# Kernel optimization log

Measured on AMD Instinct MI355X. Metric: run time of the kernel, lower is better.

Reference implementation:

```python
import jax, jax.numpy as jnp
import numpy as np
from jax.ops import segment_sum, segment_max

N_NODES = 100000
N_EDGES = 3200000
NODE_FEAT = 128
EDGE_DIM = 8
H = 4          # heads for all three layers
C_HID = 8      # out_layer_1 == out_layer_2 == 8
N_CLASSES = 1
NEG_SLOPE = 0.2


def setup_inputs() -> dict:
    key = jax.random.key(0)
    ks = jax.random.split(key, 20)
    g = lambda k, shape, fan: jax.random.normal(k, shape, jnp.float32) / np.sqrt(fan)
    inp = {
        "x": jax.random.normal(ks[0], (N_NODES, NODE_FEAT), jnp.float32),
        "edge_attr": jax.random.normal(ks[1], (N_EDGES, EDGE_DIM), jnp.float32),
        "edge_index": jax.random.randint(ks[2], (2, N_EDGES), 0, N_NODES, jnp.int32),
        # layer 1: node_feat -> H*C_HID, concat=True, with edge features
        "W1": g(ks[3], (NODE_FEAT, H * C_HID), NODE_FEAT),
        "a_src1": g(ks[4], (H, C_HID), C_HID),
        "a_dst1": g(ks[5], (H, C_HID), C_HID),
        "We1": g(ks[6], (EDGE_DIM, H * C_HID), EDGE_DIM),
        "a_e1": g(ks[7], (H, C_HID), C_HID),
        "b1": jnp.zeros((H * C_HID,), jnp.float32),
        # layer 2: H*C_HID -> C_HID, concat=False
        "W2": g(ks[8], (H * C_HID, H * C_HID), H * C_HID),
        "a_src2": g(ks[9], (H, C_HID), C_HID),
        "a_dst2": g(ks[10], (H, C_HID), C_HID),
        "b2": jnp.zeros((C_HID,), jnp.float32),
        # layer 3: C_HID -> N_CLASSES, concat=False
        "W3": g(ks[11], (C_HID, H * N_CLASSES), C_HID),
        "a_src3": g(ks[12], (H, N_CLASSES), 1),
        "a_dst3": g(ks[13], (H, N_CLASSES), 1),
        "b3": jnp.zeros((N_CLASSES,), jnp.float32),
    }
    return inp


def _gat_conv(x, src, dst, W, a_src, a_dst, bias, concat,
              edge_attr=None, W_edge=None, a_edge=None):
    """PyG GATConv forward (eval mode). src/dst already include self-loops."""
    n = x.shape[0]
    h, c = a_src.shape
    xh = (x @ W).reshape(n, h, c)                       # [N,H,C]
    alpha = (xh * a_src[None]).sum(-1)[src] \
          + (xh * a_dst[None]).sum(-1)[dst]             # [E,H]
    if edge_attr is not None:
        eh = (edge_attr @ W_edge).reshape(-1, h, c)     # [E,H,C]
        alpha = alpha + (eh * a_edge[None]).sum(-1)
    alpha = jax.nn.leaky_relu(alpha, NEG_SLOPE)
    # segment softmax over incoming edges of each dst node
    amax = segment_max(alpha, dst, num_segments=n)       # [N,H]
    ex = jnp.exp(alpha - amax[dst])
    denom = segment_sum(ex, dst, num_segments=n)
    alpha = ex / (denom[dst] + 1e-16)                    # [E,H]
    out = segment_sum(alpha[:, :, None] * xh[src], dst, num_segments=n)  # [N,H,C]
    out = out.reshape(n, h * c) if concat else out.mean(axis=1)
    return out + bias


def _add_self_loops(edge_index, n):
    loop = jnp.arange(n, dtype=edge_index.dtype)
    src = jnp.concatenate([edge_index[0], loop])
    dst = jnp.concatenate([edge_index[1], loop])
    return src, dst


def reference(x, edge_attr, edge_index, W1, a_src1, a_dst1, We1, a_e1, b1,
              W2, a_src2, a_dst2, b2, W3, a_src3, a_dst3, b3):
    n = x.shape[0]
    src, dst = _add_self_loops(edge_index, n)
    # self-loop edge_attr: fill_value='mean' => scatter-mean of edge_attr by dst
    deg = segment_sum(jnp.ones((edge_index.shape[1],), x.dtype), edge_index[1],
                      num_segments=n)
    mean_attr = segment_sum(edge_attr, edge_index[1], num_segments=n) \
              / jnp.maximum(deg, 1.0)[:, None]
    ea = jnp.concatenate([edge_attr, mean_attr], axis=0)

    h = _gat_conv(x, src, dst, W1, a_src1, a_dst1, b1, True,
                  edge_attr=ea, W_edge=We1, a_edge=a_e1)
    h = jax.nn.elu(h)
    h = _gat_conv(h, src, dst, W2, a_src2, a_dst2, b2, False)
    h = jax.nn.elu(h)
    out = _gat_conv(h, src, dst, W3, a_src3, a_dst3, b3, False)
    return out
```

## Files before the change

### kernel.cpp

```cpp
#include <hip/hip_runtime.h>
#include <hip/hip_fp16.h>
#include <cmath>

static inline int cdiv(long a, int b){ return (int)((a + b - 1) / b); }

__device__ __forceinline__ float lrelu(float x){ return x > 0.f ? x : 0.2f * x; }
__device__ __forceinline__ float elu1(float x){ return x > 0.f ? x : expm1f(x); }
__device__ __forceinline__ float fexp(float x){ return __expf(x); }
__device__ __forceinline__ float sel4(float4 v, int h){
  float ab = (h & 1) ? v.y : v.x;
  float cd = (h & 1) ? v.w : v.z;
  return (h & 2) ? cd : ab;
}

#define WAVE_FENCE() do { asm volatile("" ::: "memory"); __builtin_amdgcn_sched_barrier(0); } while(0)

#define W_SHIFT 7
#define BUCKET_N (1 << W_SHIFT)
#define NBMAX   1024
#define NCHUNKS 1024
#define CH_MAX  3136
#define MS_THREADS 1024



__global__ __launch_bounds__(MS_THREADS)
void hist_chunks_kernel(const int* __restrict__ ei, int E, int CH, int* __restrict__ hist2d){
  __shared__ int s_b[NBMAX];
  int t = threadIdx.x, chunk = blockIdx.x;
  s_b[t] = 0;
  __syncthreads();
  int lo = chunk * CH, hi = min(lo + CH, E);
  for (int e = lo + t; e < hi; e += MS_THREADS)
    atomicAdd(&s_b[ei[E + e] >> W_SHIFT], 1);
  __syncthreads();
  hist2d[(size_t)chunk * NBMAX + t] = s_b[t];
}

__global__ __launch_bounds__(NCHUNKS)
void col_scan_kernel(int* __restrict__ hist2d, int* __restrict__ bcnt){
  __shared__ int s[NCHUNKS];
  int b = blockIdx.x, t = threadIdx.x;
  int v = hist2d[(size_t)t * NBMAX + b];
  s[t] = v; __syncthreads();
  #pragma unroll
  for (int off = 1; off < NCHUNKS; off <<= 1){
    int u = (t >= off) ? s[t - off] : 0;
    __syncthreads();
    s[t] += u;
    __syncthreads();
  }
  hist2d[(size_t)t * NBMAX + b] = s[t] - v;
  if (t == NCHUNKS - 1) bcnt[b] = s[t];
}

__global__ void scan_buckets_kernel(const int* __restrict__ bcnt, int nb, int total,
                                    int* __restrict__ bstart, int* __restrict__ row_start, int n){
  __shared__ int s[1024];
  int t = threadIdx.x;
  int v = (t < nb) ? bcnt[t] : 0;
  s[t] = v; __syncthreads();
  #pragma unroll
  for (int off = 1; off < 1024; off <<= 1){
    int u = (t >= off) ? s[t - off] : 0;
    __syncthreads();
    s[t] += u;
    __syncthreads();
  }
  bstart[t] = (t < nb) ? s[t] - v : total;
  if (t == 0){ bstart[NBMAX] = total; row_start[n] = total; }
}

__global__ void wevec_kernel(const float* __restrict__ We, const float* __restrict__ ae,
                             float* __restrict__ wev){
  int i = threadIdx.x;
  if (i >= 32) return;
  int d = i >> 2, h = i & 3;
  float acc = 0.f;
  #pragma unroll
  for (int c = 0; c < 8; ++c) acc = fmaf(We[d * 32 + h * 8 + c], ae[h * 8 + c], acc);
  wev[d * 4 + h] = acc;
}

__global__ __launch_bounds__(MS_THREADS)
void multisplit_kernel(const int* __restrict__ ei, int E, int CH,
                       const float* __restrict__ eattr, const float* __restrict__ wev,
                       const int* __restrict__ bstart, const int* __restrict__ prefix2d,
                       int4* __restrict__ staged){
  __shared__ int4 s_rec[CH_MAX];
  __shared__ int s_fill[NBMAX];
  __shared__ int s_lbase[NBMAX];
  __shared__ int s_shift[NBMAX];
  __shared__ float s_wev[32];
  int t = threadIdx.x, chunk = blockIdx.x;
  if (t < 32) s_wev[t] = wev[t];
  s_fill[t] = 0;
  __syncthreads();
  int lo = chunk * CH, hi = min(lo + CH, E);
  int cnt = hi - lo;
  for (int e = lo + t; e < hi; e += MS_THREADS)
    atomicAdd(&s_fill[ei[E + e] >> W_SHIFT], 1);
  __syncthreads();
  int v = s_fill[t];
  s_lbase[t] = v; __syncthreads();
  #pragma unroll
  for (int off = 1; off < NBMAX; off <<= 1){
    int u = (t >= off) ? s_lbase[t - off] : 0;
    __syncthreads();
    s_lbase[t] += u;
    __syncthreads();
  }
  int excl = s_lbase[t] - v;
  s_lbase[t] = excl;
  s_shift[t] = bstart[t] + prefix2d[(size_t)chunk * NBMAX + t] - excl;
  s_fill[t] = 0;
  __syncthreads();
  for (int e = lo + t; e < hi; e += MS_THREADS){
    int d = ei[E + e];
    int b = d >> W_SHIFT;
    const float4* ea = (const float4*)(eattr + (size_t)e * 8);
    float4 v0 = ea[0], v1 = ea[1];
    float av[8] = {v0.x, v0.y, v0.z, v0.w, v1.x, v1.y, v1.z, v1.w};
    float e0 = 0, e1 = 0, e2 = 0, e3 = 0;
    #pragma unroll
    for (int k = 0; k < 8; ++k){
      e0 = fmaf(av[k], s_wev[k * 4 + 0], e0);
      e1 = fmaf(av[k], s_wev[k * 4 + 1], e1);
      e2 = fmaf(av[k], s_wev[k * 4 + 2], e2);
      e3 = fmaf(av[k], s_wev[k * 4 + 3], e3);
    }
    __half2 h01 = __floats2half2_rn(e0, e1);
    __half2 h23 = __floats2half2_rn(e2, e3);
    int pos = s_lbase[b] + atomicAdd(&s_fill[b], 1);
    s_rec[pos] = make_int4(ei[e], d,
                           __builtin_bit_cast(int, h01), __builtin_bit_cast(int, h23));
  }
  __syncthreads();
  for (int i = t; i < cnt; i += MS_THREADS){
    int4 r = s_rec[i];
    staged[s_shift[r.y >> W_SHIFT] + i] = r;
  }
}

__global__ __launch_bounds__(MS_THREADS)
void bucket_scatter_kernel(const int* __restrict__ bstart, const int4* __restrict__ staged,
                           int n, int* __restrict__ row_start, int* __restrict__ srcs,
                           uint2* __restrict__ escp, float4* __restrict__ selfesc){
  __shared__ int s_cnt[BUCKET_N];
  __shared__ int s_cur[BUCKET_N];
  __shared__ int s_start[BUCKET_N];
  int b = blockIdx.x, t = threadIdx.x;
  int node0 = b << W_SHIFT;
  if (t < BUCKET_N) s_cnt[t] = 0;
  __syncthreads();
  int lo = bstart[b], hi = bstart[b + 1];
  for (int i = lo + t; i < hi; i += MS_THREADS)
    atomicAdd(&s_cnt[staged[i].y & (BUCKET_N - 1)], 1);
  __syncthreads();
  if (t < BUCKET_N) s_cur[t] = s_cnt[t];
  __syncthreads();
  #pragma unroll
  for (int off = 1; off < BUCKET_N; off <<= 1){
    int v = (t < BUCKET_N && t >= off) ? s_cur[t - off] : 0;
    __syncthreads();
    if (t < BUCKET_N) s_cur[t] += v;
    __syncthreads();
  }
  if (t < BUCKET_N){
    int excl = s_cur[t] - s_cnt[t];
    int nd = node0 + t;
    if (nd <= n) row_start[nd] = lo + excl;
    s_start[t] = lo + excl;
    s_cur[t] = lo + excl;
  }
  __syncthreads();
  for (int i = lo + t; i < hi; i += MS_THREADS){
    int4 r = staged[i];
    int pos = atomicAdd(&s_cur[r.y & (BUCKET_N - 1)], 1);
    srcs[pos] = r.x;
    escp[pos] = make_uint2((unsigned)r.z, (unsigned)r.w);
  }
  __syncthreads();
  int nl = t >> 3, sub = t & 7;
  int nd2 = node0 + nl;
  if (nd2 >= n) return;
  int r0 = s_start[nl], r1 = s_start[nl] + s_cnt[nl];
  float e0 = 0, e1 = 0, e2 = 0, e3 = 0;
  for (int k = r0 + sub; k < r1; k += 8){
    uint2 u = escp[k];
    float2 f01 = __half22float2(__builtin_bit_cast(__half2, u.x));
    float2 f23 = __half22float2(__builtin_bit_cast(__half2, u.y));
    e0 += f01.x; e1 += f01.y; e2 += f23.x; e3 += f23.y;
  }
  #pragma unroll
  for (int off = 1; off < 8; off <<= 1){
    e0 += __shfl_xor(e0, off, 64); e1 += __shfl_xor(e1, off, 64);
    e2 += __shfl_xor(e2, off, 64); e3 += __shfl_xor(e3, off, 64);
  }
  if (sub == 0){
    float inv = 1.f / fmaxf((float)s_cnt[nl], 1.f);
    selfesc[nd2] = make_float4(e0 * inv, e1 * inv, e2 * inv, e3 * inv);
  }
}

template<int K, int M, int C>
__global__ void gemm_score_kernel(const float* __restrict__ A, const float* __restrict__ W,
                                  const float* __restrict__ asrc, const float* __restrict__ adst,
                                  float* __restrict__ out, float* __restrict__ sS,
                                  float* __restrict__ sD, int n){
  __shared__ float Ws[K * M];
  __shared__ float s_as[M], s_ad[M];
  for (int i = threadIdx.x; i < K * M; i += blockDim.x) Ws[i] = W[i];
  if (threadIdx.x < M){ s_as[threadIdx.x] = asrc[threadIdx.x]; s_ad[threadIdx.x] = adst[threadIdx.x]; }
  __syncthreads();
  constexpr int ROWS = 256 / M;
  int row = blockIdx.x * ROWS + (int)threadIdx.x / M;
  int col = (int)threadIdx.x % M;
  if (row >= n) return;
  const float4* a4 = (const float4*)(A + (size_t)row * K);
  float acc = 0.f;
  #pragma unroll
  for (int k4 = 0; k4 < K / 4; ++k4){
    float4 av = a4[k4];
    acc = fmaf(av.x, Ws[(k4 * 4 + 0) * M + col], acc);
    acc = fmaf(av.y, Ws[(k4 * 4 + 1) * M + col], acc);
    acc = fmaf(av.z, Ws[(k4 * 4 + 2) * M + col], acc);
    acc = fmaf(av.w, Ws[(k4 * 4 + 3) * M + col], acc);
  }
  out[(size_t)row * M + col] = acc;
  float ps = acc * s_as[col], pd = acc * s_ad[col];
  #pragma unroll
  for (int off = 1; off < C; off <<= 1){
    ps += __shfl_xor(ps, off, 64);
    pd += __shfl_xor(pd, off, 64);
  }
  if ((col & (C - 1)) == 0){
    int h = col / C;
    sS[(size_t)row * 4 + h] = ps;
    sD[(size_t)row * 4 + h] = pd;
  }
}

template<int MODE, bool EDGE>
__global__ void gather_kernel(const int* __restrict__ row_start, const int* __restrict__ srcs,
                              const uint2* __restrict__ escp, const float4* __restrict__ selfesc,
                              const float* __restrict__ sS, const float* __restrict__ sD,
                              const float* __restrict__ xh, const float* __restrict__ bias,
                              float* __restrict__ out, int n,
                              const float* __restrict__ W3p, const float* __restrict__ as3p,
                              const float* __restrict__ ad3p, float* __restrict__ xh3,
                              float* __restrict__ ss3, float* __restrict__ sd3){
  int wv = threadIdx.x >> 6, lane = threadIdx.x & 63;
  int node = blockIdx.x * 4 + wv;

  if constexpr (MODE == 2){
    if (node >= n) return;
    int rs = row_start[node], deg = row_start[node + 1] - rs;
    float4 sd4 = ((const float4*)sD)[node];
    float4 acc = {0,0,0,0}, dsum = {0,0,0,0};
    for (int k = lane; k < deg; k += 64){
      int s = srcs[rs + k];
      float4 ss = ((const float4*)sS)[s];
      float4 w;
      w.x = fexp(lrelu(ss.x + sd4.x)); w.y = fexp(lrelu(ss.y + sd4.y));
      w.z = fexp(lrelu(ss.z + sd4.z)); w.w = fexp(lrelu(ss.w + sd4.w));
      dsum.x += w.x; dsum.y += w.y; dsum.z += w.z; dsum.w += w.w;
      float4 xv = ((const float4*)xh)[s];
      acc.x = fmaf(w.x, xv.x, acc.x); acc.y = fmaf(w.y, xv.y, acc.y);
      acc.z = fmaf(w.z, xv.z, acc.z); acc.w = fmaf(w.w, xv.w, acc.w);
    }
    #pragma unroll
    for (int off = 1; off < 64; off <<= 1){
      acc.x += __shfl_xor(acc.x, off, 64); acc.y += __shfl_xor(acc.y, off, 64);
      acc.z += __shfl_xor(acc.z, off, 64); acc.w += __shfl_xor(acc.w, off, 64);
      dsum.x += __shfl_xor(dsum.x, off, 64); dsum.y += __shfl_xor(dsum.y, off, 64);
      dsum.z += __shfl_xor(dsum.z, off, 64); dsum.w += __shfl_xor(dsum.w, off, 64);
    }
    if (lane == 0){
      float4 ssn = ((const float4*)sS)[node];
      float4 wsf;
      wsf.x = fexp(lrelu(ssn.x + sd4.x)); wsf.y = fexp(lrelu(ssn.y + sd4.y));
      wsf.z = fexp(lrelu(ssn.z + sd4.z)); wsf.w = fexp(lrelu(ssn.w + sd4.w));
      float4 xvn = ((const float4*)xh)[node];
      float v = (acc.x + wsf.x * xvn.x) / (dsum.x + wsf.x + 1e-16f)
              + (acc.y + wsf.y * xvn.y) / (dsum.y + wsf.y + 1e-16f)
              + (acc.z + wsf.z * xvn.z) / (dsum.z + wsf.z + 1e-16f)
              + (acc.w + wsf.w * xvn.w) / (dsum.w + wsf.w + 1e-16f);
      out[node] = 0.25f * v + bias[0];
    }
    return;
  } else {
  __shared__ float4 s_w[4][64];
  __shared__ int    s_src[4][64];
  __shared__ float  s_w3[32];
  __shared__ float  s_a3[8];
  if constexpr (MODE == 1){
    if (threadIdx.x < 32) s_w3[threadIdx.x] = W3p[threadIdx.x];
    if (threadIdx.x < 8)
      s_a3[threadIdx.x] = (threadIdx.x < 4) ? as3p[threadIdx.x] : ad3p[threadIdx.x - 4];
    __syncthreads();
  }
  if (node >= n) return;
  int rs = row_start[node], deg = row_start[node + 1] - rs;
  float4 sd4 = ((const float4*)sD)[node];
  int q = lane & 7;
  int h = q >> 1;
  int sg = lane >> 3;
  float4 acc = {0,0,0,0};
  float dacc = 0.f;

  for (int base = 0; base < deg; base += 64){
    int k = base + lane;
    float4 w = {0,0,0,0}; int s = 0;
    if (k < deg){
      s = srcs[rs + k];
      float4 ss = ((const float4*)sS)[s];
      float a0 = ss.x + sd4.x, a1 = ss.y + sd4.y, a2 = ss.z + sd4.z, a3 = ss.w + sd4.w;
      if constexpr (EDGE){
        uint2 u = escp[rs + k];
        float2 f01 = __half22float2(__builtin_bit_cast(__half2, u.x));
        float2 f23 = __half22float2(__builtin_bit_cast(__half2, u.y));
        a0 += f01.x; a1 += f01.y; a2 += f23.x; a3 += f23.y;
      }
      w.x = fexp(lrelu(a0)); w.y = fexp(lrelu(a1));
      w.z = fexp(lrelu(a2)); w.w = fexp(lrelu(a3));
    }
    s_w[wv][lane] = w;
    s_src[wv][lane] = s;
    WAVE_FENCE();
    int nvalid = min(deg - base, 64);
    const float* s_wf = (const float*)&s_w[wv][0];
    #pragma unroll
    for (int i = 0; i < 8; ++i){
      int slot = i * 8 + sg;
      if (slot < nvalid){
        int s2 = s_src[wv][slot];
        float wg = s_wf[slot * 4 + h];
        float4 xv = ((const float4*)xh)[(size_t)s2 * 8 + q];
        dacc += wg;
        acc.x = fmaf(wg, xv.x, acc.x); acc.y = fmaf(wg, xv.y, acc.y);
        acc.z = fmaf(wg, xv.z, acc.z); acc.w = fmaf(wg, xv.w, acc.w);
      }
    }
    WAVE_FENCE();
  }

  #pragma unroll
  for (int off = 8; off < 64; off <<= 1){
    acc.x += __shfl_xor(acc.x, off, 64); acc.y += __shfl_xor(acc.y, off, 64);
    acc.z += __shfl_xor(acc.z, off, 64); acc.w += __shfl_xor(acc.w, off, 64);
    dacc  += __shfl_xor(dacc,  off, 64);
  }
  float4 ssn = ((const float4*)sS)[node];
  float a_self = sel4(ssn, h) + sel4(sd4, h);
  if constexpr (EDGE) a_self += sel4(selfesc[node], h);
  float wsel = fexp(lrelu(a_self));
  float4 xvn = ((const float4*)xh)[(size_t)node * 8 + q];
  acc.x = fmaf(wsel, xvn.x, acc.x); acc.y = fmaf(wsel, xvn.y, acc.y);
  acc.z = fmaf(wsel, xvn.z, acc.z); acc.w = fmaf(wsel, xvn.w, acc.w);
  dacc += wsel;
  float rin = 1.f / (dacc + 1e-16f);
  float4 val = {acc.x * rin, acc.y * rin, acc.z * rin, acc.w * rin};

  if constexpr (MODE == 0){
    float4 b4 = ((const float4*)bias)[q];
    val.x = elu1(val.x + b4.x); val.y = elu1(val.y + b4.y);
    val.z = elu1(val.z + b4.z); val.w = elu1(val.w + b4.w);
    if (lane < 8) ((float4*)out)[(size_t)node * 8 + lane] = val;
  } else {
    val.x += __shfl_xor(val.x, 2, 64); val.y += __shfl_xor(val.y, 2, 64);
    val.z += __shfl_xor(val.z, 2, 64); val.w += __shfl_xor(val.w, 2, 64);
    val.x += __shfl_xor(val.x, 4, 64); val.y += __shfl_xor(val.y, 4, 64);
    val.z += __shfl_xor(val.z, 4, 64); val.w += __shfl_xor(val.w, 4, 64);
    float4 b4 = ((const float4*)bias)[q & 1];
    val.x = elu1(val.x * 0.25f + b4.x); val.y = elu1(val.y * 0.25f + b4.y);
    val.z = elu1(val.z * 0.25f + b4.z); val.w = elu1(val.w * 0.25f + b4.w);
    float4 oth;
    oth.x = __shfl_xor(val.x, 1, 64); oth.y = __shfl_xor(val.y, 1, 64);
    oth.z = __shfl_xor(val.z, 1, 64); oth.w = __shfl_xor(val.w, 1, 64);
    float h2v[8];
    if (q & 1){
      h2v[0] = oth.x; h2v[1] = oth.y; h2v[2] = oth.z; h2v[3] = oth.w;
      h2v[4] = val.x; h2v[5] = val.y; h2v[6] = val.z; h2v[7] = val.w;
    } else {
      h2v[0] = val.x; h2v[1] = val.y; h2v[2] = val.z; h2v[3] = val.w;
      h2v[4] = oth.x; h2v[5] = oth.y; h2v[6] = oth.z; h2v[7] = oth.w;
    }
    float x3[4];
    #pragma unroll
    for (int j = 0; j < 4; ++j){
      float a = 0.f;
      #pragma unroll
      for (int k = 0; k < 8; ++k) a = fmaf(h2v[k], s_w3[k * 4 + j], a);
      x3[j] = a;
    }
    if (lane == 0){
      ((float4*)xh3)[node] = make_float4(x3[0], x3[1], x3[2], x3[3]);
      ((float4*)ss3)[node] = make_float4(x3[0] * s_a3[0], x3[1] * s_a3[1],
                                         x3[2] * s_a3[2], x3[3] * s_a3[3]);
      ((float4*)sd3)[node] = make_float4(x3[0] * s_a3[4], x3[1] * s_a3[5],
                                         x3[2] * s_a3[6], x3[3] * s_a3[7]);
    }
  }
  }
}


extern "C" void kernel_launch(void* const* d_in, const int* in_sizes, int n_in,
                              void* d_out, int out_size, void* d_ws, size_t ws_size,
                              hipStream_t stream){
  const float* x     = (const float*)d_in[0];
  const float* eattr = (const float*)d_in[1];
  const int*   ei    = (const int*)d_in[2];
  const float* W1  = (const float*)d_in[3];
  const float* as1 = (const float*)d_in[4];
  const float* ad1 = (const float*)d_in[5];
  const float* We1 = (const float*)d_in[6];
  const float* ae1 = (const float*)d_in[7];
  const float* b1  = (const float*)d_in[8];
  const float* W2  = (const float*)d_in[9];
  const float* as2 = (const float*)d_in[10];
  const float* ad2 = (const float*)d_in[11];
  const float* b2  = (const float*)d_in[12];
  const float* W3  = (const float*)d_in[13];
  const float* as3 = (const float*)d_in[14];
  const float* ad3 = (const float*)d_in[15];
  const float* b3  = (const float*)d_in[16];

  const int N = in_sizes[0] / 128;
  const int E = in_sizes[2] / 2;
  const int nb_buckets = (N + BUCKET_N - 1) >> W_SHIFT;
  const int CH = cdiv(E, NCHUNKS);

  char* b0 = (char*)d_ws;
  int4* staged = (int4*)b0;
  float* fp = (float*)b0;
  float* xh = fp; fp += (size_t)N * 32;
  float* sS = fp; fp += (size_t)N * 4;
  float* sD = fp; fp += (size_t)N * 4;
  float* h1 = fp; fp += (size_t)N * 32;
  int*  srcs = (int*)(b0 + (size_t)E * 16);
  uint2* escp = (uint2*)(b0 + (size_t)E * 20);
  int* hist2d = (int*)(b0 + (size_t)E * 28);
  float4* selfesc = (float4*)(hist2d + (size_t)NCHUNKS * NBMAX);
  float* xh3 = (float*)(selfesc + N);
  float* ss3 = xh3 + (size_t)N * 4;
  float* sd3 = ss3 + (size_t)N * 4;
  int* ip = (int*)(sd3 + (size_t)N * 4);
  int* bcnt      = ip; ip += NBMAX;
  int* bstart    = ip; ip += NBMAX + 1;
  int* row_start = ip; ip += N + 1;
  float* wev = (float*)ip;

  const int B = 256;

  wevec_kernel<<<1, 32, 0, stream>>>(We1, ae1, wev);
  hist_chunks_kernel<<<NCHUNKS, MS_THREADS, 0, stream>>>(ei, E, CH, hist2d);
  col_scan_kernel<<<nb_buckets, NCHUNKS, 0, stream>>>(hist2d, bcnt);
  scan_buckets_kernel<<<1, 1024, 0, stream>>>(bcnt, nb_buckets, E, bstart, row_start, N);
  multisplit_kernel<<<NCHUNKS, MS_THREADS, 0, stream>>>(ei, E, CH, eattr, wev, bstart, hist2d, staged);
  bucket_scatter_kernel<<<nb_buckets, MS_THREADS, 0, stream>>>(bstart, staged, N, row_start, srcs, escp, selfesc);

  gemm_score_kernel<128,32,8><<<cdiv(N, 8), B, 0, stream>>>(x, W1, as1, ad1, xh, sS, sD, N);
  gather_kernel<0,true><<<cdiv(N, 4), B, 0, stream>>>(row_start, srcs, escp, selfesc, sS, sD, xh, b1, h1, N,
                                                      nullptr, nullptr, nullptr, nullptr, nullptr, nullptr);

  gemm_score_kernel<32,32,8><<<cdiv(N, 8), B, 0, stream>>>(h1, W2, as2, ad2, xh, sS, sD, N);
  gather_kernel<1,false><<<cdiv(N, 4), B, 0, stream>>>(row_start, srcs, escp, selfesc, sS, sD, xh, b2, nullptr, N,
                                                       W3, as3, ad3, xh3, ss3, sd3);

  gather_kernel<2,false><<<cdiv(N, 4), B, 0, stream>>>(row_start, srcs, escp, selfesc, ss3, sd3, xh3, b3, (float*)d_out, N,
                                                       nullptr, nullptr, nullptr, nullptr, nullptr, nullptr);
}
```

Baseline: 433.6 us.

## Replace per-row GEMM+score kernel with 128-row register-tiled shared-memory GEMM

Swaps the naive one-thread-per-output GEMM for a tiled kernel. Each block stages a transposed 128-row tile of A in LDS, and each thread computes a 4x4 register tile from float4 LDS reads. This cuts redundant global loads of A rows (previously each row was read by 32 threads) and LDS traffic per FMA. The attention scores are fused into the epilogue with a single shuffle. Larger blocks mean fewer CTAs, and the LDS transpose stores may hit bank conflicts.

```diff
diff --git a/kernel.cpp b/kernel.cpp
--- a/kernel.cpp
+++ b/kernel.cpp
@@ -203,41 +203,70 @@
   }
 }
 
-template<int K, int M, int C>
-__global__ void gemm_score_kernel(const float* __restrict__ A, const float* __restrict__ W,
-                                  const float* __restrict__ asrc, const float* __restrict__ adst,
-                                  float* __restrict__ out, float* __restrict__ sS,
-                                  float* __restrict__ sD, int n){
-  __shared__ float Ws[K * M];
-  __shared__ float s_as[M], s_ad[M];
-  for (int i = threadIdx.x; i < K * M; i += blockDim.x) Ws[i] = W[i];
-  if (threadIdx.x < M){ s_as[threadIdx.x] = asrc[threadIdx.x]; s_ad[threadIdx.x] = adst[threadIdx.x]; }
-  __syncthreads();
-  constexpr int ROWS = 256 / M;
-  int row = blockIdx.x * ROWS + (int)threadIdx.x / M;
-  int col = (int)threadIdx.x % M;
-  if (row >= n) return;
-  const float4* a4 = (const float4*)(A + (size_t)row * K);
-  float acc = 0.f;
-  #pragma unroll
-  for (int k4 = 0; k4 < K / 4; ++k4){
-    float4 av = a4[k4];
-    acc = fmaf(av.x, Ws[(k4 * 4 + 0) * M + col], acc);
-    acc = fmaf(av.y, Ws[(k4 * 4 + 1) * M + col], acc);
-    acc = fmaf(av.z, Ws[(k4 * 4 + 2) * M + col], acc);
-    acc = fmaf(av.w, Ws[(k4 * 4 + 3) * M + col], acc);
-  }
-  out[(size_t)row * M + col] = acc;
-  float ps = acc * s_as[col], pd = acc * s_ad[col];
-  #pragma unroll
-  for (int off = 1; off < C; off <<= 1){
-    ps += __shfl_xor(ps, off, 64);
-    pd += __shfl_xor(pd, off, 64);
-  }
-  if ((col & (C - 1)) == 0){
-    int h = col / C;
-    sS[(size_t)row * 4 + h] = ps;
-    sD[(size_t)row * 4 + h] = pd;
+template<int K>
+__global__ __launch_bounds__(256)
+void gemm_score_tiled(const float* __restrict__ A, const float* __restrict__ W,
+                      const float* __restrict__ asrc, const float* __restrict__ adst,
+                      float* __restrict__ out, float* __restrict__ sS,
+                      float* __restrict__ sD, int n){
+  constexpr int KH = (K > 64) ? 64 : K;
+  constexpr int K4 = KH / 4;
+  __shared__ float s_AT[KH * 128];
+  __shared__ float s_W[K * 32];
+  __shared__ float s_as[32], s_ad[32];
+  int t = threadIdx.x;
+  for (int i = t; i < K * 32; i += 256) s_W[i] = W[i];
+  if (t < 32){ s_as[t] = asrc[t]; s_ad[t] = adst[t]; }
+  int n0 = blockIdx.x * 128;
+  int nrows = min(128, n - n0);
+  int rg = t >> 3, q = t & 7;
+  float4 acc[4] = {{0,0,0,0},{0,0,0,0},{0,0,0,0},{0,0,0,0}};
+
+  for (int k0 = 0; k0 < K; k0 += KH){
+    __syncthreads();
+    #pragma unroll
+    for (int it = 0; it < 128 * K4 / 256; ++it){
+      int idx = t + it * 256;
+      int row = idx & 127, k4 = idx >> 7;
+      if (row < nrows){
+        float4 v = *(const float4*)(A + (size_t)(n0 + row) * K + k0 + 4 * k4);
+        s_AT[(4 * k4 + 0) * 128 + row] = v.x;
+        s_AT[(4 * k4 + 1) * 128 + row] = v.y;
+        s_AT[(4 * k4 + 2) * 128 + row] = v.z;
+        s_AT[(4 * k4 + 3) * 128 + row] = v.w;
+      }
+    }
+    __syncthreads();
+    #pragma unroll 4
+    for (int k = 0; k < KH; ++k){
+      float4 a4 = *(const float4*)(s_AT + k * 128 + 4 * rg);
+      float4 w4 = *(const float4*)(s_W + (k0 + k) * 32 + 4 * q);
+      acc[0].x = fmaf(a4.x, w4.x, acc[0].x); acc[0].y = fmaf(a4.x, w4.y, acc[0].y);
+      acc[0].z = fmaf(a4.x, w4.z, acc[0].z); acc[0].w = fmaf(a4.x, w4.w, acc[0].w);
+      acc[1].x = fmaf(a4.y, w4.x, acc[1].x); acc[1].y = fmaf(a4.y, w4.y, acc[1].y);
+      acc[1].z = fmaf(a4.y, w4.z, acc[1].z); acc[1].w = fmaf(a4.y, w4.w, acc[1].w);
+      acc[2].x = fmaf(a4.z, w4.x, acc[2].x); acc[2].y = fmaf(a4.z, w4.y, acc[2].y);
+      acc[2].z = fmaf(a4.z, w4.z, acc[2].z); acc[2].w = fmaf(a4.z, w4.w, acc[2].w);
+      acc[3].x = fmaf(a4.w, w4.x, acc[3].x); acc[3].y = fmaf(a4.w, w4.y, acc[3].y);
+      acc[3].z = fmaf(a4.w, w4.z, acc[3].z); acc[3].w = fmaf(a4.w, w4.w, acc[3].w);
+    }
+  }
+
+  float as0 = s_as[4 * q + 0], as1 = s_as[4 * q + 1], as2 = s_as[4 * q + 2], as3 = s_as[4 * q + 3];
+  float ad0 = s_ad[4 * q + 0], ad1 = s_ad[4 * q + 1], ad2 = s_ad[4 * q + 2], ad3 = s_ad[4 * q + 3];
+  #pragma unroll
+  for (int i = 0; i < 4; ++i){
+    int row = n0 + 4 * rg + i;
+    bool ok = (4 * rg + i) < nrows;
+    if (ok) ((float4*)out)[(size_t)row * 8 + q] = acc[i];
+    float ps = acc[i].x * as0 + acc[i].y * as1 + acc[i].z * as2 + acc[i].w * as3;
+    float pd = acc[i].x * ad0 + acc[i].y * ad1 + acc[i].z * ad2 + acc[i].w * ad3;
+    ps += __shfl_xor(ps, 1, 64);
+    pd += __shfl_xor(pd, 1, 64);
+    if (ok && !(q & 1)){
+      sS[(size_t)row * 4 + (q >> 1)] = ps;
+      sD[(size_t)row * 4 + (q >> 1)] = pd;
+    }
   }
 }
 
@@ -461,11 +490,11 @@
   multisplit_kernel<<<NCHUNKS, MS_THREADS, 0, stream>>>(ei, E, CH, eattr, wev, bstart, hist2d, staged);
   bucket_scatter_kernel<<<nb_buckets, MS_THREADS, 0, stream>>>(bstart, staged, N, row_start, srcs, escp, selfesc);
 
-  gemm_score_kernel<128,32,8><<<cdiv(N, 8), B, 0, stream>>>(x, W1, as1, ad1, xh, sS, sD, N);
+  gemm_score_tiled<128><<<cdiv(N, 128), B, 0, stream>>>(x, W1, as1, ad1, xh, sS, sD, N);
   gather_kernel<0,true><<<cdiv(N, 4), B, 0, stream>>>(row_start, srcs, escp, selfesc, sS, sD, xh, b1, h1, N,
                                                       nullptr, nullptr, nullptr, nullptr, nullptr, nullptr);
 
-  gemm_score_kernel<32,32,8><<<cdiv(N, 8), B, 0, stream>>>(h1, W2, as2, ad2, xh, sS, sD, N);
+  gemm_score_tiled<32><<<cdiv(N, 128), B, 0, stream>>>(h1, W2, as2, ad2, xh, sS, sD, N);
   gather_kernel<1,false><<<cdiv(N, 4), B, 0, stream>>>(row_start, srcs, escp, selfesc, sS, sD, xh, b2, nullptr, N,
                                                        W3, as3, ad3, xh3, ss3, sd3);
 
```

Result: faster. 385.8 us (-11.0%).
